# Kernel optimization log

Hardware: AMD Instinct MI355X
Metric: run time of the kernel (lower is better)

The kernel has to match this reference:

```python
import jax, jax.numpy as jnp
import numpy as np


def setup_inputs() -> dict:
    key = jax.random.key(0)
    ks = jax.random.split(key, 5)
    B, N, Fin, Fout = 8, 2048, 512, 512
    stdv = 1.0 / np.sqrt(Fout)
    w_stdv = 1.0 / np.sqrt(Fin)
    x = jax.random.normal(ks[0], (B, N, Fin), dtype=jnp.float32)
    weight = jax.random.uniform(ks[1], (Fin, Fout), dtype=jnp.float32, minval=-stdv, maxval=stdv)
    bias = jax.random.uniform(ks[2], (Fout,), dtype=jnp.float32, minval=-stdv, maxval=stdv)
    w_one = jax.random.uniform(ks[3], (Fin, Fin), dtype=jnp.float32, minval=-w_stdv, maxval=w_stdv)
    w_two = jax.random.uniform(ks[4], (Fin, Fin), dtype=jnp.float32, minval=-w_stdv, maxval=w_stdv)
    return {"x": x, "weight": weight, "bias": bias, "w_one": w_one, "w_two": w_two}


def reference(x, weight, bias, w_one, w_two):
    # x: [B, N, Fin]
    support = jnp.einsum('bnf,fo->bno', x, weight)          # [B, N, Fout]
    phi_one = jnp.einsum('ef,bnf->ben', w_one, x)           # [B, Fin, N]
    phi_two = jnp.einsum('ef,bnf->ben', w_two, x)           # [B, Fin, N]
    adj = jnp.einsum('ben,bem->bnm', phi_one, phi_two)      # [B, N, N]
    adj = jax.nn.softmax(adj, axis=1)                        # softmax over dim=1 (columns)
    out = jnp.einsum('bnm,bmo->bno', adj, support)           # [B, N, Fout]
    return out + bias
```

## Files before the change

### kernel.cpp

```cpp
#include <hip/hip_runtime.h>
#include <math.h>

#define BB 8
#define NN 2048
#define FF 512
#define LOG2E 1.4426950408889634f

typedef __attribute__((ext_vector_type(8))) short short8;
typedef __attribute__((ext_vector_type(4))) float floatx4;
typedef __attribute__((ext_vector_type(2))) float float2v;
typedef __attribute__((ext_vector_type(2))) __bf16 bf16x2;

__device__ __forceinline__ unsigned short f2bf(float f) {
    union { float f; unsigned u; } v; v.f = f;
    unsigned r = v.u + 0x7FFFu + ((v.u >> 16) & 1u);
    return (unsigned short)(r >> 16);
}

__device__ __forceinline__ float fexp2(float x) {
#if __has_builtin(__builtin_amdgcn_exp2f)
    return __builtin_amdgcn_exp2f(x);
#else
    return __expf(x * 0.69314718056f);
#endif
}

__device__ __forceinline__ void pk_store(unsigned short* p0, unsigned short* p1,
                                         float a, float b) {
    union { bf16x2 h; unsigned short s[2]; } u;
    float2v v; v.x = a; v.y = b;
    u.h = __builtin_convertvector(v, bf16x2);
    *p0 = u.s[0]; *p1 = u.s[1];
}

__global__ __launch_bounds__(128, 2) void gemm_bt16(
    const unsigned short* __restrict__ A, const unsigned short* __restrict__ B,
    void* __restrict__ Cv, const float* __restrict__ bias, float* __restrict__ Dsum,
    int K, int a_ld, int b_ld, int ldc,
    long a_batch, long b_batch, long c_batch, int mode)
{
    __shared__ __align__(16) unsigned short Alds[128 * 64];
    __shared__ __align__(16) unsigned short Blds[128 * 64];

    const int tid  = threadIdx.x;
    const int wave = tid >> 6;
    const int lane = tid & 63;
    const int bz   = blockIdx.z;

    const int m0 = blockIdx.y * 128;
    const int n0 = blockIdx.x * 128;

    const unsigned short* Aptr = A + (long)bz * a_batch + (long)m0 * a_ld;
    const unsigned short* Bptr = B + (long)bz * b_batch + (long)n0 * b_ld;

    const int wn   = wave * 64;
    const int fl   = lane & 15;
    const int quad = lane >> 4;

    int offA[8], offB[8];
    #pragma unroll
    for (int s = 0; s < 8; ++s) {
        const int c = s * 128 + tid;
        const int row = c >> 3;
        const int kq = ((c & 7) ^ (row & 7)) << 3;
        offA[s] = row * a_ld + kq;
        offB[s] = row * b_ld + kq;
    }

    floatx4 acc[8][4] = {};

    for (int k0 = 0; k0 < K; k0 += 64) {
        #pragma unroll
        for (int s = 0; s < 8; ++s) {
            __builtin_amdgcn_global_load_lds(
                (const __attribute__((address_space(1))) void*)(Aptr + offA[s]),
                (__attribute__((address_space(3))) void*)&Alds[(s * 128 + tid - lane) * 8], 16, 0, 0);
            __builtin_amdgcn_global_load_lds(
                (const __attribute__((address_space(1))) void*)(Bptr + offB[s]),
                (__attribute__((address_space(3))) void*)&Blds[(s * 128 + tid - lane) * 8], 16, 0, 0);
        }
        Aptr += 64; Bptr += 64;
        __syncthreads();

        #pragma unroll
        for (int s = 0; s < 2; ++s) {
            const int slot = ((s * 4 + quad) ^ (fl & 7)) * 8;
            short8 af[8], bf[4];
            #pragma unroll
            for (int j = 0; j < 4; ++j)
                bf[j] = *(const short8*)&Blds[(wn + j * 16 + fl) * 64 + slot];
            #pragma unroll
            for (int i = 0; i < 8; ++i)
                af[i] = *(const short8*)&Alds[(i * 16 + fl) * 64 + slot];
            #pragma unroll
            for (int i = 0; i < 8; ++i)
                #pragma unroll
                for (int j = 0; j < 4; ++j)
                    acc[i][j] = __builtin_amdgcn_mfma_f32_16x16x32_bf16(af[i], bf[j], acc[i][j], 0, 0, 0);
        }
        __syncthreads();
    }

    if (mode == 0) {
        float* Cb = (float*)Cv + (long)bz * c_batch;
        #pragma unroll
        for (int j = 0; j < 4; ++j) {
            const int ng = n0 + wn + j * 16 + fl;
            const float badd = bias ? bias[ng] : 0.0f;
            #pragma unroll
            for (int i = 0; i < 8; ++i) {
                const int mg = m0 + i * 16 + quad * 4;
                #pragma unroll
                for (int r = 0; r < 4; ++r)
                    Cb[(long)(mg + r) * ldc + ng] = acc[i][j][r] + badd;
            }
        }
    } else if (mode == 1) {
        unsigned short* Cb = (unsigned short*)Cv + (long)bz * c_batch;
        #pragma unroll
        for (int j = 0; j < 4; ++j) {
            const int ng = n0 + wn + j * 16 + fl;
            #pragma unroll
            for (int i = 0; i < 8; ++i) {
                const int mg = m0 + i * 16 + quad * 4;
                pk_store(&Cb[(long)(mg + 0) * ldc + ng], &Cb[(long)(mg + 1) * ldc + ng],
                         acc[i][j][0], acc[i][j][1]);
                pk_store(&Cb[(long)(mg + 2) * ldc + ng], &Cb[(long)(mg + 3) * ldc + ng],
                         acc[i][j][2], acc[i][j][3]);
            }
        }
    } else {
        unsigned short* Cb = (unsigned short*)Cv + (long)bz * c_batch;
        float* Db = Dsum + (long)bz * NN;
        #pragma unroll
        for (int i = 0; i < 8; ++i)
            #pragma unroll
            for (int j = 0; j < 4; ++j)
                #pragma unroll
                for (int r = 0; r < 4; ++r)
                    acc[i][j][r] = fexp2(acc[i][j][r]);
        #pragma unroll
        for (int j = 0; j < 4; ++j) {
            const int ng = n0 + wn + j * 16 + fl;
            float csum = 0.f;
            #pragma unroll
            for (int i = 0; i < 8; ++i) {
                const int mg = m0 + i * 16 + quad * 4;
                csum += acc[i][j][0] + acc[i][j][1] + acc[i][j][2] + acc[i][j][3];
                pk_store(&Cb[(long)(mg + 0) * ldc + ng], &Cb[(long)(mg + 1) * ldc + ng],
                         acc[i][j][0], acc[i][j][1]);
                pk_store(&Cb[(long)(mg + 2) * ldc + ng], &Cb[(long)(mg + 3) * ldc + ng],
                         acc[i][j][2], acc[i][j][3]);
            }
            csum += __shfl_xor(csum, 16);
            csum += __shfl_xor(csum, 32);
            if (quad == 0) atomicAdd(&Db[ng], csum);
        }
    }
}

__global__ __launch_bounds__(256) void convert_all(
    const float* __restrict__ x, const float* __restrict__ w1, const float* __restrict__ w2,
    unsigned short* __restrict__ xb, unsigned short* __restrict__ w1b, unsigned short* __restrict__ w2b)
{
    const long NX = (long)BB * NN * FF / 8;
    const long NW = (long)FF * FF / 8;
    long t = (long)blockIdx.x * 256 + threadIdx.x;
    const float* in; unsigned short* out; float sc = 1.0f;
    if (t < NX) { in = x; out = xb; }
    else if (t < NX + NW) { in = w1; out = w1b; t -= NX; sc = LOG2E; }
    else if (t < NX + 2 * NW) { in = w2; out = w2b; t -= NX + NW; }
    else return;
    const long i = t * 8;
    float4 a = *(const float4*)(in + i);
    float4 b = *(const float4*)(in + i + 4);
    union { bf16x2 h[4]; short8 s8; } u;
    float2v v;
    v.x = a.x * sc; v.y = a.y * sc; u.h[0] = __builtin_convertvector(v, bf16x2);
    v.x = a.z * sc; v.y = a.w * sc; u.h[1] = __builtin_convertvector(v, bf16x2);
    v.x = b.x * sc; v.y = b.y * sc; u.h[2] = __builtin_convertvector(v, bf16x2);
    v.x = b.z * sc; v.y = b.w * sc; u.h[3] = __builtin_convertvector(v, bf16x2);
    *(short8*)(out + i) = u.s8;
}

__global__ __launch_bounds__(256) void transpose_convert(
    const float* __restrict__ in, unsigned short* __restrict__ out, int dim)
{
    __shared__ float t[32][33];
    const int tx = threadIdx.x & 31, ty = threadIdx.x >> 5;
    const int x0 = blockIdx.x * 32, y0 = blockIdx.y * 32;
    #pragma unroll
    for (int k = 0; k < 32; k += 8)
        t[ty + k][tx] = in[(long)(y0 + ty + k) * dim + x0 + tx];
    __syncthreads();
    #pragma unroll
    for (int k = 0; k < 32; k += 8)
        out[(long)(x0 + ty + k) * dim + y0 + tx] = f2bf(t[tx][ty + k]);
}

__global__ __launch_bounds__(256) void zero_f32(float* __restrict__ p, long n)
{
    long i = (long)blockIdx.x * 256 + threadIdx.x;
    if (i < n) p[i] = 0.0f;
}

__global__ __launch_bounds__(256) void scale_transpose(
    const unsigned short* __restrict__ Call, const float* __restrict__ D,
    unsigned short* __restrict__ supT, int batch0)
{
    __shared__ float t[32][33];
    __shared__ float rD[32];
    const int tx = threadIdx.x & 31, ty = threadIdx.x >> 5;
    const int mt = blockIdx.x * 32, ot = blockIdx.y * 32;
    const int b = batch0 + blockIdx.z;
    const unsigned short* Cb = Call + (long)b * NN * 1536;
    unsigned short* Tb = supT + (long)b * NN * FF;
    if (threadIdx.x < 32) rD[threadIdx.x] = 1.0f / D[(long)b * NN + mt + threadIdx.x];
    __syncthreads();
    #pragma unroll
    for (int k = 0; k < 32; k += 8) {
        unsigned short u = Cb[(long)(mt + ty + k) * 1536 + 1024 + ot + tx];
        union { unsigned uu; float f; } cv; cv.uu = ((unsigned)u) << 16;
        t[ty + k][tx] = cv.f;
    }
    __syncthreads();
    #pragma unroll
    for (int k = 0; k < 32; k += 8)
        Tb[(long)(ot + ty + k) * NN + mt + tx] = f2bf(t[tx][ty + k] * rD[tx]);
}

extern "C" void kernel_launch(void* const* d_in, const int* in_sizes, int n_in,
                              void* d_out, int out_size, void* d_ws, size_t ws_size,
                              hipStream_t stream)
{
    const float* x      = (const float*)d_in[0];
    const float* weight = (const float*)d_in[1];
    const float* bias   = (const float*)d_in[2];
    const float* w_one  = (const float*)d_in[3];
    const float* w_two  = (const float*)d_in[4];
    float* out = (float*)d_out;

    const long NF  = (long)NN * FF;
    const long NN2 = (long)NN * NN;
    const long CROW = 1536;

    char* p = (char*)d_ws;
    unsigned short* xb    = (unsigned short*)p; p += (size_t)BB * NF * 2;
    unsigned short* Wall  = (unsigned short*)p; p += (size_t)CROW * FF * 2;
    unsigned short* Call  = (unsigned short*)p; p += (size_t)BB * NN * CROW * 2;
    unsigned short* supT  = (unsigned short*)p; p += (size_t)BB * NF * 2;
    float*          Dsum  = (float*)p;          p += (size_t)BB * NN * 4;
    unsigned short* E     = (unsigned short*)p;
    unsigned short* w1b = Wall;
    unsigned short* w2b = Wall + (size_t)FF * FF;
    unsigned short* wTb = Wall + (size_t)2 * FF * FF;

    const size_t fixed = (size_t)(p - (char*)d_ws);
    const bool full = ws_size >= fixed + (size_t)BB * NN2 * 2;

    dim3 blk(256);
    dim3 gblk(128);

    convert_all<<<dim3(4352), blk, 0, stream>>>(x, w_one, w_two, xb, w1b, w2b);
    transpose_convert<<<dim3(FF / 32, FF / 32), blk, 0, stream>>>(weight, wTb, FF);
    zero_f32<<<dim3((BB * NN) / 256), blk, 0, stream>>>(Dsum, BB * NN);

    gemm_bt16<<<dim3(CROW / 128, NN / 128, BB), gblk, 0, stream>>>(
        xb, Wall, Call, nullptr, nullptr, FF,
        FF, FF, (int)CROW, NF, 0, NN * CROW, 1);

    if (full) {
        gemm_bt16<<<dim3(NN / 128, NN / 128, BB), gblk, 0, stream>>>(
            Call, Call + FF, E, nullptr, Dsum, FF,
            (int)CROW, (int)CROW, NN, NN * CROW, NN * CROW, NN2, 2);
        scale_transpose<<<dim3(NN / 32, FF / 32, BB), blk, 0, stream>>>(Call, Dsum, supT, 0);
        gemm_bt16<<<dim3(FF / 128, NN / 128, BB), gblk, 0, stream>>>(
            E, supT, out, bias, nullptr, NN,
            NN, NN, FF, NN2, NF, NF, 0);
    } else {
        for (int b = 0; b < BB; ++b) {
            const unsigned short* Cb = Call + (size_t)b * NN * CROW;
            gemm_bt16<<<dim3(NN / 128, NN / 128, 1), gblk, 0, stream>>>(
                Cb, Cb + FF, E, nullptr, Dsum + (size_t)b * NN, FF,
                (int)CROW, (int)CROW, NN, 0, 0, 0, 2);
            scale_transpose<<<dim3(NN / 32, FF / 32, 1), blk, 0, stream>>>(Call, Dsum, supT, b);
            gemm_bt16<<<dim3(FF / 128, NN / 128, 1), gblk, 0, stream>>>(
                E, supT + (size_t)b * NF, out + (size_t)b * NF, bias, nullptr, NN,
                NN, NN, FF, 0, 0, 0, 0);
        }
    }
}
```

Measured before the change: 242.6 us.

## Fold w_one and w_two into one Gram matrix to shrink the projection GEMM

The two projection weights are precomputed into a single 512x512 product G = w2^T·w1, scaled by log2e. The first GEMM then produces x·G and x·W, two 512-column blocks instead of three. The score GEMM multiplies that projected block against raw xb. This cuts projection FLOPs and Call memory by a third, at the cost of a small extra GEMM and the bf16 rounding of G. The convert and zero kernels are also merged to remove launches.

```diff
diff --git a/kernel.cpp b/kernel.cpp
--- a/kernel.cpp
+++ b/kernel.cpp
@@ -4,6 +4,7 @@
 #define BB 8
 #define NN 2048
 #define FF 512
+#define CROW 1024
 #define LOG2E 1.4426950408889634f
 
 typedef __attribute__((ext_vector_type(8))) short short8;
@@ -43,7 +44,6 @@
     __shared__ __align__(16) unsigned short Blds[128 * 64];
 
     const int tid  = threadIdx.x;
-    const int wave = tid >> 6;
     const int lane = tid & 63;
     const int bz   = blockIdx.z;
 
@@ -53,7 +53,7 @@
     const unsigned short* Aptr = A + (long)bz * a_batch + (long)m0 * a_ld;
     const unsigned short* Bptr = B + (long)bz * b_batch + (long)n0 * b_ld;
 
-    const int wn   = wave * 64;
+    const int wn   = (tid >> 6) * 64;
     const int fl   = lane & 15;
     const int quad = lane >> 4;
 
@@ -159,49 +159,44 @@
     }
 }
 
-__global__ __launch_bounds__(256) void convert_all(
-    const float* __restrict__ x, const float* __restrict__ w1, const float* __restrict__ w2,
-    unsigned short* __restrict__ xb, unsigned short* __restrict__ w1b, unsigned short* __restrict__ w2b)
-{
-    const long NX = (long)BB * NN * FF / 8;
-    const long NW = (long)FF * FF / 8;
-    long t = (long)blockIdx.x * 256 + threadIdx.x;
-    const float* in; unsigned short* out; float sc = 1.0f;
-    if (t < NX) { in = x; out = xb; }
-    else if (t < NX + NW) { in = w1; out = w1b; t -= NX; sc = LOG2E; }
-    else if (t < NX + 2 * NW) { in = w2; out = w2b; t -= NX + NW; }
-    else return;
+__global__ __launch_bounds__(256) void convert_x(
+    const float* __restrict__ x, unsigned short* __restrict__ xb,
+    float* __restrict__ Dsum)
+{
+    const long t = (long)blockIdx.x * 256 + threadIdx.x;
+    if (t < BB * NN) Dsum[t] = 0.0f;
     const long i = t * 8;
-    float4 a = *(const float4*)(in + i);
-    float4 b = *(const float4*)(in + i + 4);
+    float4 a = *(const float4*)(x + i);
+    float4 b = *(const float4*)(x + i + 4);
     union { bf16x2 h[4]; short8 s8; } u;
     float2v v;
-    v.x = a.x * sc; v.y = a.y * sc; u.h[0] = __builtin_convertvector(v, bf16x2);
-    v.x = a.z * sc; v.y = a.w * sc; u.h[1] = __builtin_convertvector(v, bf16x2);
-    v.x = b.x * sc; v.y = b.y * sc; u.h[2] = __builtin_convertvector(v, bf16x2);
-    v.x = b.z * sc; v.y = b.w * sc; u.h[3] = __builtin_convertvector(v, bf16x2);
-    *(short8*)(out + i) = u.s8;
-}
-
-__global__ __launch_bounds__(256) void transpose_convert(
-    const float* __restrict__ in, unsigned short* __restrict__ out, int dim)
+    v.x = a.x; v.y = a.y; u.h[0] = __builtin_convertvector(v, bf16x2);
+    v.x = a.z; v.y = a.w; u.h[1] = __builtin_convertvector(v, bf16x2);
+    v.x = b.x; v.y = b.y; u.h[2] = __builtin_convertvector(v, bf16x2);
+    v.x = b.z; v.y = b.w; u.h[3] = __builtin_convertvector(v, bf16x2);
+    *(short8*)(xb + i) = u.s8;
+}
+
+__global__ __launch_bounds__(256) void transpose3(
+    const float* __restrict__ w1, const float* __restrict__ w2,
+    const float* __restrict__ wgt,
+    unsigned short* __restrict__ w1T, unsigned short* __restrict__ w2T,
+    unsigned short* __restrict__ wT)
 {
     __shared__ float t[32][33];
     const int tx = threadIdx.x & 31, ty = threadIdx.x >> 5;
     const int x0 = blockIdx.x * 32, y0 = blockIdx.y * 32;
+    const float* in; unsigned short* out; float sc = 1.0f;
+    if (blockIdx.z == 0) { in = w1; out = w1T; sc = LOG2E; }
+    else if (blockIdx.z == 1) { in = w2; out = w2T; }
+    else { in = wgt; out = wT; }
     #pragma unroll
     for (int k = 0; k < 32; k += 8)
-        t[ty + k][tx] = in[(long)(y0 + ty + k) * dim + x0 + tx];
+        t[ty + k][tx] = in[(long)(y0 + ty + k) * FF + x0 + tx];
     __syncthreads();
     #pragma unroll
     for (int k = 0; k < 32; k += 8)
-        out[(long)(x0 + ty + k) * dim + y0 + tx] = f2bf(t[tx][ty + k]);
-}
-
-__global__ __launch_bounds__(256) void zero_f32(float* __restrict__ p, long n)
-{
-    long i = (long)blockIdx.x * 256 + threadIdx.x;
-    if (i < n) p[i] = 0.0f;
+        out[(long)(x0 + ty + k) * FF + y0 + tx] = f2bf(t[tx][ty + k] * sc);
 }
 
 __global__ __launch_bounds__(256) void scale_transpose(
@@ -213,13 +208,13 @@
     const int tx = threadIdx.x & 31, ty = threadIdx.x >> 5;
     const int mt = blockIdx.x * 32, ot = blockIdx.y * 32;
     const int b = batch0 + blockIdx.z;
-    const unsigned short* Cb = Call + (long)b * NN * 1536;
+    const unsigned short* Cb = Call + (long)b * NN * CROW;
     unsigned short* Tb = supT + (long)b * NN * FF;
     if (threadIdx.x < 32) rD[threadIdx.x] = 1.0f / D[(long)b * NN + mt + threadIdx.x];
     __syncthreads();
     #pragma unroll
     for (int k = 0; k < 32; k += 8) {
-        unsigned short u = Cb[(long)(mt + ty + k) * 1536 + 1024 + ot + tx];
+        unsigned short u = Cb[(long)(mt + ty + k) * CROW + 512 + ot + tx];
         union { unsigned uu; float f; } cv; cv.uu = ((unsigned)u) << 16;
         t[ty + k][tx] = cv.f;
     }
@@ -242,18 +237,18 @@
 
     const long NF  = (long)NN * FF;
     const long NN2 = (long)NN * NN;
-    const long CROW = 1536;
 
     char* p = (char*)d_ws;
     unsigned short* xb    = (unsigned short*)p; p += (size_t)BB * NF * 2;
-    unsigned short* Wall  = (unsigned short*)p; p += (size_t)CROW * FF * 2;
+    unsigned short* w1T   = (unsigned short*)p; p += (size_t)FF * FF * 2;
+    unsigned short* w2T   = (unsigned short*)p; p += (size_t)FF * FF * 2;
+    unsigned short* Wall2 = (unsigned short*)p; p += (size_t)CROW * FF * 2;
     unsigned short* Call  = (unsigned short*)p; p += (size_t)BB * NN * CROW * 2;
     unsigned short* supT  = (unsigned short*)p; p += (size_t)BB * NF * 2;
     float*          Dsum  = (float*)p;          p += (size_t)BB * NN * 4;
     unsigned short* E     = (unsigned short*)p;
-    unsigned short* w1b = Wall;
-    unsigned short* w2b = Wall + (size_t)FF * FF;
-    unsigned short* wTb = Wall + (size_t)2 * FF * FF;
+    unsigned short* Gt = Wall2;
+    unsigned short* wT = Wall2 + (size_t)FF * FF;
 
     const size_t fixed = (size_t)(p - (char*)d_ws);
     const bool full = ws_size >= fixed + (size_t)BB * NN2 * 2;
@@ -261,28 +256,29 @@
     dim3 blk(256);
     dim3 gblk(128);
 
-    convert_all<<<dim3(4352), blk, 0, stream>>>(x, w_one, w_two, xb, w1b, w2b);
-    transpose_convert<<<dim3(FF / 32, FF / 32), blk, 0, stream>>>(weight, wTb, FF);
-    zero_f32<<<dim3((BB * NN) / 256), blk, 0, stream>>>(Dsum, BB * NN);
+    convert_x<<<dim3(4096), blk, 0, stream>>>(x, xb, Dsum);
+    transpose3<<<dim3(16, 16, 3), blk, 0, stream>>>(w_one, w_two, weight, w1T, w2T, wT);
+
+    gemm_bt16<<<dim3(4, 4, 1), gblk, 0, stream>>>(
+        w2T, w1T, Gt, nullptr, nullptr, FF, FF, FF, FF, 0, 0, 0, 1);
 
     gemm_bt16<<<dim3(CROW / 128, NN / 128, BB), gblk, 0, stream>>>(
-        xb, Wall, Call, nullptr, nullptr, FF,
-        FF, FF, (int)CROW, NF, 0, NN * CROW, 1);
+        xb, Wall2, Call, nullptr, nullptr, FF,
+        FF, FF, CROW, NF, 0, (long)NN * CROW, 1);
 
     if (full) {
         gemm_bt16<<<dim3(NN / 128, NN / 128, BB), gblk, 0, stream>>>(
-            Call, Call + FF, E, nullptr, Dsum, FF,
-            (int)CROW, (int)CROW, NN, NN * CROW, NN * CROW, NN2, 2);
+            Call, xb, E, nullptr, Dsum, FF,
+            CROW, FF, NN, (long)NN * CROW, NF, NN2, 2);
         scale_transpose<<<dim3(NN / 32, FF / 32, BB), blk, 0, stream>>>(Call, Dsum, supT, 0);
         gemm_bt16<<<dim3(FF / 128, NN / 128, BB), gblk, 0, stream>>>(
             E, supT, out, bias, nullptr, NN,
             NN, NN, FF, NN2, NF, NF, 0);
     } else {
         for (int b = 0; b < BB; ++b) {
-            const unsigned short* Cb = Call + (size_t)b * NN * CROW;
             gemm_bt16<<<dim3(NN / 128, NN / 128, 1), gblk, 0, stream>>>(
-                Cb, Cb + FF, E, nullptr, Dsum + (size_t)b * NN, FF,
-                (int)CROW, (int)CROW, NN, 0, 0, 0, 2);
+                Call + (size_t)b * NN * CROW, xb + (size_t)b * NF, E, nullptr,
+                Dsum + (size_t)b * NN, FF, CROW, FF, NN, 0, 0, 0, 2);
             scale_transpose<<<dim3(NN / 32, FF / 32, 1), blk, 0, stream>>>(Call, Dsum, supT, b);
             gemm_bt16<<<dim3(FF / 128, NN / 128, 1), gblk, 0, stream>>>(
                 E, supT + (size_t)b * NF, out + (size_t)b * NF, bias, nullptr, NN,
```

Result: no change. 243.6 us (+0.4%).
